# Optimization experiments

Measured on AMD Instinct MI355X. Metric: run time of the kernel, lower is better.

Reference implementation:

```python
import math
import jax, jax.numpy as jnp
import numpy as np

VERY_NEGATIVE_NUMBER = -1e29
HEADS = 16
UNITS = 1024
INPUT_DIM = 1024
B, LQ, LK = 2, 2048, 2048


def setup_inputs() -> dict:
    key = jax.random.key(0)
    ks = jax.random.split(key, 8)
    s = 1.0 / math.sqrt(INPUT_DIM)
    return {
        "query": jax.random.normal(ks[0], (B, LQ, INPUT_DIM), jnp.float32),
        "key": jax.random.normal(ks[1], (B, LK, INPUT_DIM), jnp.float32),
        "value": jax.random.normal(ks[2], (B, LK, INPUT_DIM), jnp.float32),
        "key_mask": jax.random.randint(ks[3], (B, LK), 0, 2, jnp.int32),
        "Wq": jax.random.normal(ks[4], (INPUT_DIM, UNITS), jnp.float32) * s,
        "bq": jnp.zeros((UNITS,), jnp.float32),
        "Wk": jax.random.normal(ks[5], (INPUT_DIM, UNITS), jnp.float32) * s,
        "bk": jnp.zeros((UNITS,), jnp.float32),
        "Wv": jax.random.normal(ks[6], (INPUT_DIM, UNITS), jnp.float32) * s,
        "bv": jnp.zeros((UNITS,), jnp.float32),
    }


def reference(query, key, value, key_mask, Wq, bq, Wk, bk, Wv, bv):
    b, lq, lk = query.shape[0], query.shape[1], key.shape[1]
    h = HEADS
    d = UNITS // h  # head dim
    # projections -> [B, L, H, D]
    wq = (query @ Wq + bq).reshape(b, lq, h, d)
    wk = (key @ Wk + bk).reshape(b, lk, h, d)
    wv = (value @ Wv + bv).reshape(b, lk, h, d)
    scale = 1.0 / math.sqrt(float(UNITS) / h)
    # scores laid out [H, B, Q, K] as in the torch code
    scores = jnp.einsum("bqhd,bkhd->hbqk", wq, wk) * scale
    # additive key mask, broadcast [1, B, 1, K]
    km = key_mask.astype(scores.dtype)
    scores = scores + (1.0 - km)[None, :, None, :] * VERY_NEGATIVE_NUMBER
    sim = jax.nn.softmax(scores, axis=-1)
    out = jnp.einsum("hbqk,bkhd->bqhd", sim, wv).reshape(b, lq, UNITS)
    return out
```

## Files before the change

### kernel.cpp

```cpp
#include <hip/hip_runtime.h>
#include <cstdint>
#include <cstddef>

typedef __attribute__((ext_vector_type(4))) float f32x4;
typedef __attribute__((ext_vector_type(8))) short bf16x8;
typedef __attribute__((ext_vector_type(4))) unsigned int u32x4;

#define QSCALE 0.18033688011112042f
#define NSHIFT 17.3123404906676f

static __device__ __forceinline__ unsigned short f2bf(float f) {
    return (unsigned short)((__builtin_bit_cast(unsigned int, f) + 0x8000u) >> 16);
}
static __device__ __forceinline__ unsigned int pk2(float a, float b) {
    unsigned int ua = __builtin_bit_cast(unsigned int, a) + 0x8000u;
    unsigned int ub = __builtin_bit_cast(unsigned int, b) + 0x8000u;
    return (ua >> 16) | (ub & 0xffff0000u);
}
static __device__ __forceinline__ unsigned int pack2h(float a, float b) {
    unsigned int ua = __builtin_bit_cast(unsigned int, a) + 0x8000u;
    unsigned int ub = __builtin_bit_cast(unsigned int, b) + 0x8000u;
    return __builtin_amdgcn_perm(ub, ua, 0x07060302);
}
static __device__ __forceinline__ void glds16(const unsigned short* g, unsigned short* l) {
    __builtin_amdgcn_global_load_lds((const __attribute__((address_space(1))) void*)g,
                                     (__attribute__((address_space(3))) void*)l, 16, 0, 0);
}

__global__ __launch_bounds__(256) void prep(
    const float* __restrict__ Wq, const float* __restrict__ Wk, const float* __restrict__ Wv,
    const float* __restrict__ Xq, const float* __restrict__ Xk, const float* __restrict__ Xv,
    unsigned short* __restrict__ Wt, unsigned short* __restrict__ Xb)
{
    const int z = blockIdx.y;
    if (blockIdx.x < 1024) {
        __shared__ float tile[32][33];
        const float* W = (z == 0) ? Wq : (z == 1) ? Wk : Wv;
        unsigned short* dst = Wt + (size_t)z * 1048576;
        int n0 = (blockIdx.x & 31) * 32, k0 = (blockIdx.x >> 5) * 32;
        int tx = threadIdx.x & 31, ty = threadIdx.x >> 5;
#pragma unroll
        for (int i = 0; i < 32; i += 8)
            tile[ty + i][tx] = W[(size_t)(k0 + ty + i) * 1024 + n0 + tx];
        __syncthreads();
#pragma unroll
        for (int i = 0; i < 32; i += 8)
            dst[(size_t)(n0 + ty + i) * 1024 + k0 + tx] = f2bf(tile[tx][ty + i]);
    } else {
        const float* X = (z == 0) ? Xq : (z == 1) ? Xk : Xv;
        unsigned short* dst = Xb + (size_t)z * 4194304;
        size_t base = (size_t)(blockIdx.x - 1024) * 2048 + threadIdx.x * 8;
        float4 a = *(const float4*)&X[base];
        float4 c = *(const float4*)&X[base + 4];
        *(int4*)&dst[base] = make_int4(pk2(a.x, a.y), pk2(a.z, a.w),
                                       pk2(c.x, c.y), pk2(c.z, c.w));
    }
}

__global__ __launch_bounds__(256, 3) void proj_g(
    const unsigned short* __restrict__ Xb, const unsigned short* __restrict__ Wt,
    const float* __restrict__ bq, const float* __restrict__ bk, const float* __restrict__ bv,
    const int* __restrict__ km, unsigned short* __restrict__ packs)
{
    const int mode = blockIdx.z;
    const unsigned short* X = Xb + (size_t)mode * 4194304;
    const unsigned short* W = Wt + (size_t)mode * 1048576;
    const float* bias = (mode == 0) ? bq : (mode == 1) ? bk : bv;
    unsigned short* outp = packs + (size_t)mode * 4194304;

    __shared__ alignas(16) unsigned short As[128 * 64];
    __shared__ alignas(16) unsigned short Bs[128 * 64];

    const int tid = threadIdx.x, wid = tid >> 6, lane = tid & 63;
    const int lrow = lane & 15, g = lane >> 4;
    const int m0 = blockIdx.x * 128, n0 = blockIdx.y * 128;
    const int wr = (wid >> 1) * 64, wc = (wid & 1) * 64;
    const int srow = tid >> 3;
    const int scol = ((tid & 7) ^ (srow & 7)) * 8;
    const int sdst = srow * 64 + (tid & 7) * 8;

    f32x4 acc[4][4] = {};

    for (int k0 = 0; k0 < 1024; k0 += 64) {
        __syncthreads();
#pragma unroll
        for (int p = 0; p < 4; ++p)
            glds16(&X[(size_t)(m0 + p * 32 + srow) * 1024 + k0 + scol], &As[p * 2048 + sdst]);
#pragma unroll
        for (int p = 0; p < 4; ++p)
            glds16(&W[(size_t)(n0 + p * 32 + srow) * 1024 + k0 + scol], &Bs[p * 2048 + sdst]);
        asm volatile("s_waitcnt vmcnt(0)" ::: "memory");
        __syncthreads();

#pragma unroll
        for (int kk = 0; kk < 2; ++kk) {
            bf16x8 af[4], bfr[4];
#pragma unroll
            for (int i = 0; i < 4; ++i)
                af[i] = *(const bf16x8*)&As[(wr + i * 16 + lrow) * 64 + (((kk * 4 + g) ^ (lrow & 7)) * 8)];
#pragma unroll
            for (int j = 0; j < 4; ++j)
                bfr[j] = *(const bf16x8*)&Bs[(wc + j * 16 + lrow) * 64 + (((kk * 4 + g) ^ (lrow & 7)) * 8)];
#pragma unroll
            for (int i = 0; i < 4; ++i)
#pragma unroll
                for (int j = 0; j < 4; ++j)
                    acc[i][j] = __builtin_amdgcn_mfma_f32_16x16x32_bf16(af[i], bfr[j], acc[i][j], 0, 0, 0);
        }
    }

#pragma unroll
    for (int j = 0; j < 4; ++j) {
        int n = n0 + wc + j * 16 + lrow;
        float bv_ = bias[n];
        int h = n >> 6, d = n & 63;
#pragma unroll
        for (int i = 0; i < 4; ++i) {
#pragma unroll
            for (int r = 0; r < 4; ++r) {
                int m = m0 + wr + i * 16 + g * 4 + r;
                float val = acc[i][j][r] + bv_;
                if (mode == 0) val *= QSCALE;
                int b = m >> 11, l = m & 2047;
                size_t idx;
                if (mode == 2) {
                    val *= (float)km[m];
                    idx = (((size_t)((b << 4) + h) << 6) + d) * 2048 + l;
                } else {
                    idx = (((size_t)((b << 4) + h) << 11) + l) * 64 + d;
                }
                outp[idx] = f2bf(val);
            }
        }
    }
}

__global__ __launch_bounds__(256) void transpose_w3(
    const float* __restrict__ Wq, const float* __restrict__ Wk,
    const float* __restrict__ Wv, unsigned short* __restrict__ Wt)
{
    __shared__ float tile[32][33];
    const float* W = (blockIdx.z == 0) ? Wq : (blockIdx.z == 1) ? Wk : Wv;
    unsigned short* dst = Wt + (size_t)blockIdx.z * 1048576;
    int tx = threadIdx.x & 31, ty = threadIdx.x >> 5;
    int n0 = blockIdx.x * 32, k0 = blockIdx.y * 32;
#pragma unroll
    for (int i = 0; i < 32; i += 8)
        tile[ty + i][tx] = W[(size_t)(k0 + ty + i) * 1024 + n0 + tx];
    __syncthreads();
#pragma unroll
    for (int i = 0; i < 32; i += 8)
        dst[(size_t)(n0 + ty + i) * 1024 + k0 + tx] = f2bf(tile[tx][ty + i]);
}

__global__ __launch_bounds__(256, 3) void proj_fb(
    const float* __restrict__ Xq, const float* __restrict__ Xk, const float* __restrict__ Xv,
    const unsigned short* __restrict__ Wt,
    const float* __restrict__ bq, const float* __restrict__ bk, const float* __restrict__ bv,
    const int* __restrict__ km, unsigned short* __restrict__ packs)
{
    const int mode = blockIdx.z;
    const float* X = (mode == 0) ? Xq : (mode == 1) ? Xk : Xv;
    const unsigned short* W = Wt + (size_t)mode * 1048576;
    const float* bias = (mode == 0) ? bq : (mode == 1) ? bk : bv;
    unsigned short* outp = packs + (size_t)mode * 4194304;

    __shared__ alignas(16) unsigned short As[128 * 64];
    __shared__ alignas(16) unsigned short Bs[128 * 64];

    const int tid = threadIdx.x, wid = tid >> 6, lane = tid & 63;
    const int lrow = lane & 15, g = lane >> 4;
    const int m0 = blockIdx.x * 128, n0 = blockIdx.y * 128;
    const int wr = (wid >> 1) * 64, wc = (wid & 1) * 64;
    const int srow = tid >> 3;
    const int scol = ((tid & 7) ^ (srow & 7)) * 8;
    const int sdst = srow * 64 + (tid & 7) * 8;
    const int ar = tid >> 2;
    const int acb = (tid & 3) * 2;

    f32x4 acc[4][4] = {};

    for (int k0 = 0; k0 < 1024; k0 += 64) {
        __syncthreads();
#pragma unroll
        for (int p = 0; p < 4; ++p)
            glds16(&W[(size_t)(n0 + p * 32 + srow) * 1024 + k0 + scol], &Bs[p * 2048 + sdst]);
#pragma unroll
        for (int p = 0; p < 2; ++p) {
            int r = p * 64 + ar;
#pragma unroll
            for (int bl = 0; bl < 2; ++bl) {
                int cb = acb + bl;
                const float* src = &X[(size_t)(m0 + r) * 1024 + k0 + cb * 8];
                float4 v0 = *(const float4*)src;
                float4 v1 = *(const float4*)(src + 4);
                *(int4*)&As[r * 64 + ((cb ^ (r & 7)) * 8)] =
                    make_int4(pk2(v0.x, v0.y), pk2(v0.z, v0.w),
                              pk2(v1.x, v1.y), pk2(v1.z, v1.w));
            }
        }
        asm volatile("s_waitcnt vmcnt(0)" ::: "memory");
        __syncthreads();

#pragma unroll
        for (int kk = 0; kk < 2; ++kk) {
            bf16x8 af[4], bfr[4];
#pragma unroll
            for (int i = 0; i < 4; ++i)
                af[i] = *(const bf16x8*)&As[(wr + i * 16 + lrow) * 64 + (((kk * 4 + g) ^ (lrow & 7)) * 8)];
#pragma unroll
            for (int j = 0; j < 4; ++j)
                bfr[j] = *(const bf16x8*)&Bs[(wc + j * 16 + lrow) * 64 + (((kk * 4 + g) ^ (lrow & 7)) * 8)];
#pragma unroll
            for (int i = 0; i < 4; ++i)
#pragma unroll
                for (int j = 0; j < 4; ++j)
                    acc[i][j] = __builtin_amdgcn_mfma_f32_16x16x32_bf16(af[i], bfr[j], acc[i][j], 0, 0, 0);
        }
    }

#pragma unroll
    for (int j = 0; j < 4; ++j) {
        int n = n0 + wc + j * 16 + lrow;
        float bv_ = bias[n];
        int h = n >> 6, d = n & 63;
#pragma unroll
        for (int i = 0; i < 4; ++i) {
#pragma unroll
            for (int r = 0; r < 4; ++r) {
                int m = m0 + wr + i * 16 + g * 4 + r;
                float val = acc[i][j][r] + bv_;
                if (mode == 0) val *= QSCALE;
                int b = m >> 11, l = m & 2047;
                size_t idx;
                if (mode == 2) {
                    val *= (float)km[m];
                    idx = (((size_t)((b << 4) + h) << 6) + d) * 2048 + l;
                } else {
                    idx = (((size_t)((b << 4) + h) << 11) + l) * 64 + d;
                }
                outp[idx] = f2bf(val);
            }
        }
    }
}

__global__ __launch_bounds__(256, 4) void attn(
    const unsigned short* __restrict__ Qp, const unsigned short* __restrict__ Kp,
    const unsigned short* __restrict__ Vtp, const int* __restrict__ km_g,
    float* __restrict__ out)
{
    __shared__ alignas(16) unsigned short Ks[2][4096];
    __shared__ alignas(16) unsigned short Vs[2][4096];
    __shared__ alignas(16) unsigned short Ms[2048];

    const int tid = threadIdx.x, wid = tid >> 6, lane = tid & 63;
    const int lrow = lane & 15, g = lane >> 4;
    const int bh = blockIdx.y, b = bh >> 4, h = bh & 15;
    const int q0 = blockIdx.x * 64;
    const unsigned short* Q = Qp + (size_t)bh * 131072;
    const unsigned short* K = Kp + (size_t)bh * 131072;
    const unsigned short* V = Vtp + (size_t)bh * 131072;

    const int sr = lane >> 3;
    const int sc = ((lane & 7) ^ sr) * 8;
    const int sw = (lane & 7) * 8;

    {
        const int* km = km_g + b * 2048;
        int4 a = *(const int4*)&km[tid * 8];
        int4 c = *(const int4*)&km[tid * 8 + 4];
        unsigned int w0 = (a.x ? 0x3F80u : 0u) | ((a.y ? 0x3F80u : 0u) << 16);
        unsigned int w1 = (a.z ? 0x3F80u : 0u) | ((a.w ? 0x3F80u : 0u) << 16);
        unsigned int w2 = (c.x ? 0x3F80u : 0u) | ((c.y ? 0x3F80u : 0u) << 16);
        unsigned int w3 = (c.z ? 0x3F80u : 0u) | ((c.w ? 0x3F80u : 0u) << 16);
        *(int4*)&Ms[tid * 8] = make_int4(w0, w1, w2, w3);
    }

    const unsigned short* qrow = Q + (size_t)(q0 + wid * 16 + lrow) * 64;
    bf16x8 qf0 = *(const bf16x8*)(qrow + g * 8);
    bf16x8 qf1 = *(const bf16x8*)(qrow + 32 + g * 8);

    const int vr0 = wid * 16 + sr, vr1 = vr0 + 8;
    const int pk0 = ((vr0 >> 4) & 1) * 32 + ((vr0 >> 2) & 3) * 8 + ((vr0 >> 5) & 1) * 4 + (vr0 & 3);
    const int pk1 = ((vr1 >> 4) & 1) * 32 + ((vr1 >> 2) & 3) * 8 + ((vr1 >> 5) & 1) * 4 + (vr1 & 3);

    auto STAGE = [&](int buf, int kt) {
        glds16(&K[(size_t)(kt + pk0) * 64 + sc], &Ks[buf][vr0 * 64 + sw]);
        glds16(&K[(size_t)(kt + pk1) * 64 + sc], &Ks[buf][vr1 * 64 + sw]);
        glds16(&V[(size_t)vr0 * 2048 + kt + sc], &Vs[buf][vr0 * 64 + sw]);
        glds16(&V[(size_t)vr1 * 2048 + kt + sc], &Vs[buf][vr1 * 64 + sw]);
    };

    f32x4 accO[4] = {};
    f32x4 accL = {};
    const f32x4 sinit = {-NSHIFT, -NSHIFT, -NSHIFT, -NSHIFT};

    STAGE(0, 0);
    for (int t = 0; t < 32; ++t) {
        const int cur = t & 1, kt = t * 64;
        asm volatile("s_waitcnt vmcnt(0)" ::: "memory");
        __syncthreads();
        if (t < 31) STAGE(cur ^ 1, kt + 64);

        bf16x8 mf0 = *(const bf16x8*)&Ms[kt + g * 8];
        bf16x8 mf1 = *(const bf16x8*)&Ms[kt + 32 + g * 8];

        f32x4 accS[4];
#pragma unroll
        for (int s = 0; s < 4; ++s) {
            const int krow = s * 16 + lrow;
            bf16x8 kf0 = *(const bf16x8*)&Ks[cur][krow * 64 + ((g ^ (lrow & 7)) * 8)];
            bf16x8 kf1 = *(const bf16x8*)&Ks[cur][krow * 64 + (((4 + g) ^ (lrow & 7)) * 8)];
            accS[s] = __builtin_amdgcn_mfma_f32_16x16x32_bf16(kf0, qf0, sinit, 0, 0, 0);
            accS[s] = __builtin_amdgcn_mfma_f32_16x16x32_bf16(kf1, qf1, accS[s], 0, 0, 0);
        }

        float e0[4], e1[4], e2[4], e3[4];
#pragma unroll
        for (int r = 0; r < 4; ++r) {
            e0[r] = exp2f(accS[0][r]);
            e1[r] = exp2f(accS[1][r]);
            e2[r] = exp2f(accS[2][r]);
            e3[r] = exp2f(accS[3][r]);
        }
        u32x4 t0 = {pack2h(e0[0], e0[1]), pack2h(e0[2], e0[3]),
                    pack2h(e2[0], e2[1]), pack2h(e2[2], e2[3])};
        u32x4 t1 = {pack2h(e1[0], e1[1]), pack2h(e1[2], e1[3]),
                    pack2h(e3[0], e3[1]), pack2h(e3[2], e3[3])};
        bf16x8 pf0 = __builtin_bit_cast(bf16x8, t0);
        bf16x8 pf1 = __builtin_bit_cast(bf16x8, t1);

        accL = __builtin_amdgcn_mfma_f32_16x16x32_bf16(pf0, mf0, accL, 0, 0, 0);
        accL = __builtin_amdgcn_mfma_f32_16x16x32_bf16(pf1, mf1, accL, 0, 0, 0);
#pragma unroll
        for (int j = 0; j < 4; ++j) {
            bf16x8 vf0 = *(const bf16x8*)&Vs[cur][(j * 16 + lrow) * 64 + ((g ^ (lrow & 7)) * 8)];
            bf16x8 vf1 = *(const bf16x8*)&Vs[cur][(j * 16 + lrow) * 64 + (((4 + g) ^ (lrow & 7)) * 8)];
            accO[j] = __builtin_amdgcn_mfma_f32_16x16x32_bf16(pf0, vf0, accO[j], 0, 0, 0);
            accO[j] = __builtin_amdgcn_mfma_f32_16x16x32_bf16(pf1, vf1, accO[j], 0, 0, 0);
        }
    }

#pragma unroll
    for (int j = 0; j < 4; ++j) {
#pragma unroll
        for (int r = 0; r < 4; ++r) {
            int qq = q0 + wid * 16 + g * 4 + r;
            out[((size_t)(b * 2048 + qq)) * 1024 + h * 64 + j * 16 + lrow] = accO[j][r] / accL[r];
        }
    }
}

extern "C" void kernel_launch(void* const* d_in, const int* in_sizes, int n_in,
                              void* d_out, int out_size, void* d_ws, size_t ws_size,
                              hipStream_t stream) {
    const float* query    = (const float*)d_in[0];
    const float* key      = (const float*)d_in[1];
    const float* value    = (const float*)d_in[2];
    const int*   key_mask = (const int*)d_in[3];
    const float* Wq = (const float*)d_in[4];
    const float* bq = (const float*)d_in[5];
    const float* Wk = (const float*)d_in[6];
    const float* bk = (const float*)d_in[7];
    const float* Wv = (const float*)d_in[8];
    const float* bv = (const float*)d_in[9];
    float* out = (float*)d_out;

    char* ws = (char*)d_ws;
    unsigned short* Wt = (unsigned short*)ws;
    unsigned short* Pk = (unsigned short*)(ws + 6291456);
    unsigned short* Xb = (unsigned short*)(ws + 31457280);

    if (ws_size >= 56623104ull) {
        prep<<<dim3(3072, 3), 256, 0, stream>>>(Wq, Wk, Wv, query, key, value, Wt, Xb);
        proj_g<<<dim3(32, 8, 3), 256, 0, stream>>>(Xb, Wt, bq, bk, bv, key_mask, Pk);
    } else {
        transpose_w3<<<dim3(32, 32, 3), 256, 0, stream>>>(Wq, Wk, Wv, Wt);
        proj_fb<<<dim3(32, 8, 3), 256, 0, stream>>>(query, key, value, Wt, bq, bk, bv, key_mask, Pk);
    }
    attn<<<dim3(32, 32), 256, 0, stream>>>(Pk, Pk + 4194304, Pk + 8388608, key_mask, out);
}
```

Measured before the change: 125.1 us.

## Enlarge attention tile to 128 queries and 128 keys per stage

```diff
diff --git a/kernel.cpp b/kernel.cpp
--- a/kernel.cpp
+++ b/kernel.cpp
@@ -245,19 +245,19 @@
     }
 }
 
-__global__ __launch_bounds__(256, 4) void attn(
+__global__ __launch_bounds__(256, 2) void attn(
     const unsigned short* __restrict__ Qp, const unsigned short* __restrict__ Kp,
     const unsigned short* __restrict__ Vtp, const int* __restrict__ km_g,
     float* __restrict__ out)
 {
-    __shared__ alignas(16) unsigned short Ks[2][4096];
-    __shared__ alignas(16) unsigned short Vs[2][4096];
+    __shared__ alignas(16) unsigned short Ks[2][128 * 64];
+    __shared__ alignas(16) unsigned short Vs[2][64 * 128];
     __shared__ alignas(16) unsigned short Ms[2048];
 
     const int tid = threadIdx.x, wid = tid >> 6, lane = tid & 63;
     const int lrow = lane & 15, g = lane >> 4;
     const int bh = blockIdx.y, b = bh >> 4, h = bh & 15;
-    const int q0 = blockIdx.x * 64;
+    const int q0 = blockIdx.x * 128;
     const unsigned short* Q = Qp + (size_t)bh * 131072;
     const unsigned short* K = Kp + (size_t)bh * 131072;
     const unsigned short* V = Vtp + (size_t)bh * 131072;
@@ -277,79 +277,114 @@
         *(int4*)&Ms[tid * 8] = make_int4(w0, w1, w2, w3);
     }
 
-    const unsigned short* qrow = Q + (size_t)(q0 + wid * 16 + lrow) * 64;
-    bf16x8 qf0 = *(const bf16x8*)(qrow + g * 8);
-    bf16x8 qf1 = *(const bf16x8*)(qrow + 32 + g * 8);
-
-    const int vr0 = wid * 16 + sr, vr1 = vr0 + 8;
-    const int pk0 = ((vr0 >> 4) & 1) * 32 + ((vr0 >> 2) & 3) * 8 + ((vr0 >> 5) & 1) * 4 + (vr0 & 3);
-    const int pk1 = ((vr1 >> 4) & 1) * 32 + ((vr1 >> 2) & 3) * 8 + ((vr1 >> 5) & 1) * 4 + (vr1 & 3);
+    bf16x8 qf[2][2];
+#pragma unroll
+    for (int qs = 0; qs < 2; ++qs) {
+        const unsigned short* qrow = Q + (size_t)(q0 + wid * 32 + qs * 16 + lrow) * 64;
+        qf[qs][0] = *(const bf16x8*)(qrow + g * 8);
+        qf[qs][1] = *(const bf16x8*)(qrow + 32 + g * 8);
+    }
+
+    const int kr0 = wid * 16 + sr, kr1 = kr0 + 8;
+    const int pk0 = ((kr0 >> 4) & 1) * 32 + ((kr0 >> 2) & 3) * 8 + ((kr0 >> 5) & 1) * 4 + (kr0 & 3);
+    const int pk1 = ((kr1 >> 4) & 1) * 32 + ((kr1 >> 2) & 3) * 8 + ((kr1 >> 5) & 1) * 4 + (kr1 & 3);
 
     auto STAGE = [&](int buf, int kt) {
-        glds16(&K[(size_t)(kt + pk0) * 64 + sc], &Ks[buf][vr0 * 64 + sw]);
-        glds16(&K[(size_t)(kt + pk1) * 64 + sc], &Ks[buf][vr1 * 64 + sw]);
-        glds16(&V[(size_t)vr0 * 2048 + kt + sc], &Vs[buf][vr0 * 64 + sw]);
-        glds16(&V[(size_t)vr1 * 2048 + kt + sc], &Vs[buf][vr1 * 64 + sw]);
+#pragma unroll
+        for (int c = 0; c < 2; ++c) {
+            glds16(&K[(size_t)(kt + c * 64 + pk0) * 64 + sc], &Ks[buf][(c * 64 + kr0) * 64 + sw]);
+            glds16(&K[(size_t)(kt + c * 64 + pk1) * 64 + sc], &Ks[buf][(c * 64 + kr1) * 64 + sw]);
+        }
+#pragma unroll
+        for (int i = 0; i < 4; ++i) {
+            const int dbase = wid * 16 + i * 4;
+            const int d = dbase + (lane >> 4);
+            const int vc = (lane >> 3) & 1;
+            const int b8 = lane & 7;
+            glds16(&V[(size_t)d * 2048 + kt + vc * 64 + ((b8 ^ (d & 7)) * 8)],
+                   &Vs[buf][dbase * 128 + lane * 8]);
+        }
     };
 
-    f32x4 accO[4] = {};
-    f32x4 accL = {};
+    f32x4 accO[2][4] = {};
+    f32x4 accL[2] = {};
     const f32x4 sinit = {-NSHIFT, -NSHIFT, -NSHIFT, -NSHIFT};
 
     STAGE(0, 0);
-    for (int t = 0; t < 32; ++t) {
-        const int cur = t & 1, kt = t * 64;
+    for (int t = 0; t < 16; ++t) {
+        const int cur = t & 1, kt = t * 128;
         asm volatile("s_waitcnt vmcnt(0)" ::: "memory");
         __syncthreads();
-        if (t < 31) STAGE(cur ^ 1, kt + 64);
-
-        bf16x8 mf0 = *(const bf16x8*)&Ms[kt + g * 8];
-        bf16x8 mf1 = *(const bf16x8*)&Ms[kt + 32 + g * 8];
-
-        f32x4 accS[4];
-#pragma unroll
-        for (int s = 0; s < 4; ++s) {
-            const int krow = s * 16 + lrow;
-            bf16x8 kf0 = *(const bf16x8*)&Ks[cur][krow * 64 + ((g ^ (lrow & 7)) * 8)];
-            bf16x8 kf1 = *(const bf16x8*)&Ks[cur][krow * 64 + (((4 + g) ^ (lrow & 7)) * 8)];
-            accS[s] = __builtin_amdgcn_mfma_f32_16x16x32_bf16(kf0, qf0, sinit, 0, 0, 0);
-            accS[s] = __builtin_amdgcn_mfma_f32_16x16x32_bf16(kf1, qf1, accS[s], 0, 0, 0);
-        }
-
-        float e0[4], e1[4], e2[4], e3[4];
-#pragma unroll
-        for (int r = 0; r < 4; ++r) {
-            e0[r] = exp2f(accS[0][r]);
-            e1[r] = exp2f(accS[1][r]);
-            e2[r] = exp2f(accS[2][r]);
-            e3[r] = exp2f(accS[3][r]);
-        }
-        u32x4 t0 = {pack2h(e0[0], e0[1]), pack2h(e0[2], e0[3]),
-                    pack2h(e2[0], e2[1]), pack2h(e2[2], e2[3])};
-        u32x4 t1 = {pack2h(e1[0], e1[1]), pack2h(e1[2], e1[3]),
-                    pack2h(e3[0], e3[1]), pack2h(e3[2], e3[3])};
-        bf16x8 pf0 = __builtin_bit_cast(bf16x8, t0);
-        bf16x8 pf1 = __builtin_bit_cast(bf16x8, t1);
-
-        accL = __builtin_amdgcn_mfma_f32_16x16x32_bf16(pf0, mf0, accL, 0, 0, 0);
-        accL = __builtin_amdgcn_mfma_f32_16x16x32_bf16(pf1, mf1, accL, 0, 0, 0);
-#pragma unroll
-        for (int j = 0; j < 4; ++j) {
-            bf16x8 vf0 = *(const bf16x8*)&Vs[cur][(j * 16 + lrow) * 64 + ((g ^ (lrow & 7)) * 8)];
-            bf16x8 vf1 = *(const bf16x8*)&Vs[cur][(j * 16 + lrow) * 64 + (((4 + g) ^ (lrow & 7)) * 8)];
-            accO[j] = __builtin_amdgcn_mfma_f32_16x16x32_bf16(pf0, vf0, accO[j], 0, 0, 0);
-            accO[j] = __builtin_amdgcn_mfma_f32_16x16x32_bf16(pf1, vf1, accO[j], 0, 0, 0);
-        }
-    }
-
-#pragma unroll
-    for (int j = 0; j < 4; ++j) {
-#pragma unroll
-        for (int r = 0; r < 4; ++r) {
-            int qq = q0 + wid * 16 + g * 4 + r;
-            out[((size_t)(b * 2048 + qq)) * 1024 + h * 64 + j * 16 + lrow] = accO[j][r] / accL[r];
-        }
-    }
+        if (t < 15) STAGE(cur ^ 1, kt + 128);
+
+#pragma unroll
+        for (int half = 0; half < 2; ++half) {
+            const int kb = half * 64;
+
+            f32x4 accS[2][4];
+#pragma unroll
+            for (int s = 0; s < 4; ++s) {
+                const int krow = kb + s * 16 + lrow;
+                bf16x8 kf0 = *(const bf16x8*)&Ks[cur][krow * 64 + ((g ^ (lrow & 7)) * 8)];
+                bf16x8 kf1 = *(const bf16x8*)&Ks[cur][krow * 64 + (((4 + g) ^ (lrow & 7)) * 8)];
+#pragma unroll
+                for (int qs = 0; qs < 2; ++qs) {
+                    accS[qs][s] = __builtin_amdgcn_mfma_f32_16x16x32_bf16(kf0, qf[qs][0], sinit, 0, 0, 0);
+                    accS[qs][s] = __builtin_amdgcn_mfma_f32_16x16x32_bf16(kf1, qf[qs][1], accS[qs][s], 0, 0, 0);
+                }
+            }
+
+            bf16x8 pf[2][2];
+#pragma unroll
+            for (int qs = 0; qs < 2; ++qs) {
+                float e0[4], e1[4], e2[4], e3[4];
+#pragma unroll
+                for (int r = 0; r < 4; ++r) {
+                    e0[r] = exp2f(accS[qs][0][r]);
+                    e1[r] = exp2f(accS[qs][1][r]);
+                    e2[r] = exp2f(accS[qs][2][r]);
+                    e3[r] = exp2f(accS[qs][3][r]);
+                }
+                u32x4 t0 = {pack2h(e0[0], e0[1]), pack2h(e0[2], e0[3]),
+                            pack2h(e2[0], e2[1]), pack2h(e2[2], e2[3])};
+                u32x4 t1 = {pack2h(e1[0], e1[1]), pack2h(e1[2], e1[3]),
+                            pack2h(e3[0], e3[1]), pack2h(e3[2], e3[3])};
+                pf[qs][0] = __builtin_bit_cast(bf16x8, t0);
+                pf[qs][1] = __builtin_bit_cast(bf16x8, t1);
+            }
+
+            bf16x8 mf0 = *(const bf16x8*)&Ms[kt + kb + g * 8];
+            bf16x8 mf1 = *(const bf16x8*)&Ms[kt + kb + 32 + g * 8];
+#pragma unroll
+            for (int qs = 0; qs < 2; ++qs) {
+                accL[qs] = __builtin_amdgcn_mfma_f32_16x16x32_bf16(pf[qs][0], mf0, accL[qs], 0, 0, 0);
+                accL[qs] = __builtin_amdgcn_mfma_f32_16x16x32_bf16(pf[qs][1], mf1, accL[qs], 0, 0, 0);
+            }
+
+#pragma unroll
+            for (int j = 0; j < 4; ++j) {
+                const int vrow = (j * 16 + lrow) * 128 + kb;
+                bf16x8 vf0 = *(const bf16x8*)&Vs[cur][vrow + ((g ^ (lrow & 7)) * 8)];
+                bf16x8 vf1 = *(const bf16x8*)&Vs[cur][vrow + (((4 + g) ^ (lrow & 7)) * 8)];
+#pragma unroll
+                for (int qs = 0; qs < 2; ++qs) {
+                    accO[qs][j] = __builtin_amdgcn_mfma_f32_16x16x32_bf16(pf[qs][0], vf0, accO[qs][j], 0, 0, 0);
+                    accO[qs][j] = __builtin_amdgcn_mfma_f32_16x16x32_bf16(pf[qs][1], vf1, accO[qs][j], 0, 0, 0);
+                }
+            }
+        }
+    }
+
+#pragma unroll
+    for (int qs = 0; qs < 2; ++qs)
+#pragma unroll
+        for (int j = 0; j < 4; ++j)
+#pragma unroll
+            for (int r = 0; r < 4; ++r) {
+                int qq = q0 + wid * 32 + qs * 16 + g * 4 + r;
+                out[((size_t)(b * 2048 + qq)) * 1024 + h * 64 + j * 16 + lrow] =
+                    accO[qs][j][r] / accL[qs][r];
+            }
 }
 
 extern "C" void kernel_launch(void* const* d_in, const int* in_sizes, int n_in,
@@ -379,5 +414,5 @@
         transpose_w3<<<dim3(32, 32, 3), 256, 0, stream>>>(Wq, Wk, Wv, Wt);
         proj_fb<<<dim3(32, 8, 3), 256, 0, stream>>>(query, key, value, Wt, bq, bk, bv, key_mask, Pk);
     }
-    attn<<<dim3(32, 32), 256, 0, stream>>>(Pk, Pk + 4194304, Pk + 8388608, key_mask, out);
-}
+    attn<<<dim3(16, 32), 256, 0, stream>>>(Pk, Pk + 4194304, Pk + 8388608, key_mask, out);
+}
```

After: 126.8 us. Within noise of the previous version (+1.3%).
